# Performance work log

Measured on AMD Instinct MI355X. Metric: run time of the kernel, lower is better.

## Reference

```python
import jax, jax.numpy as jnp
import numpy as np

B, F, O = 32, 26, 20
IN, G = 2048, 512
REL = 53
EPS = 1e-5  # BatchNorm1d default eps


def setup_inputs() -> dict:
    key = jax.random.key(0)
    ks = jax.random.split(key, 10)
    inp = {
        "region_feats": jax.random.normal(ks[0], (B, F, O, IN), jnp.float32),
        "region_masks": jnp.ones((B, F, O), jnp.float32),
        "rel_feats": jax.random.randint(ks[1], (B, F, O, O), 0, REL, jnp.int64),
        "tem_feats": jax.random.uniform(ks[2], (B, F * O, F * O), jnp.float32),
        # learned params (eval mode: dropout off, BN uses running stats)
        "rel_W": jax.random.normal(ks[3], (G, IN), jnp.float32) * (1.0 / np.sqrt(IN)),
        "rel_b": jnp.zeros((G,), jnp.float32),
        "rel_emb": jax.random.normal(ks[4], (REL, G), jnp.float32) * 0.02,
        "tem_W": jax.random.normal(ks[5], (G, IN), jnp.float32) * (1.0 / np.sqrt(IN)),
        "tem_b": jnp.zeros((G,), jnp.float32),
        "bn_w": jnp.ones((F * O,), jnp.float32),
        "bn_b": jnp.zeros((F * O,), jnp.float32),
        "bn_rm": jnp.zeros((F * O,), jnp.float32),
        "bn_rv": jnp.ones((F * O,), jnp.float32),
    }
    return inp


def reference(region_feats, region_masks, rel_feats, tem_feats,
              rel_W, rel_b, rel_emb, tem_W, tem_b,
              bn_w, bn_b, bn_rm, bn_rv):
    b, f, o, _ = region_feats.shape
    # ---- RELATIONAL FEATURE GRAPH ----
    # [B,F,O,G]
    rel_region = jnp.einsum("bfoi,gi->bfog", region_feats, rel_W) + rel_b
    # embedding lookup: [B,F,O,O,G]
    emb = rel_emb[rel_feats]
    mask = (rel_feats > 0).astype(region_feats.dtype)  # [B,F,O,O]
    msum = jnp.sum(mask, axis=3)                        # [B,F,O]
    # sum_j mask_ij * emb_ij  (masked reduction over neighbor dim)
    emb_sum = jnp.einsum("bfijg,bfij->bfig", emb, mask)
    # sum_j mask_ij * r_i == r_i * msum_i, so (emb_sum + r*msum)/msum
    rel_out = (emb_sum + rel_region * msum[..., None]) / msum[..., None]
    rel_out = rel_out.reshape(b, f * o, -1)
    # ---- TEMPORAL FEATURE GRAPH ----
    tem_region = jnp.einsum("bfoi,gi->bfog", region_feats, tem_W) + tem_b
    tem_region = tem_region.reshape(b, f * o, -1)
    tem_sum = jnp.sum(tem_feats, axis=2)                # [B, F*O]
    tem_out = jnp.matmul(tem_feats, tem_region) / tem_sum[..., None]
    # ---- OUTPUT ----
    out = jnp.concatenate([rel_out, tem_out], axis=-1)  # [B, F*O, 2G]
    out = jnp.tanh(out)
    # BatchNorm1d over channel dim 1 (eval mode, running stats)
    inv = bn_w / jnp.sqrt(bn_rv + EPS)                  # [F*O]
    out = (out - bn_rm[None, :, None]) * inv[None, :, None] + bn_b[None, :, None]
    return out
```

## Files before the change

kernel.cpp:

```cpp
#include <hip/hip_runtime.h>
#include <stdint.h>

#define BB 32
#define FO 520
#define M1 16640
#define KIN 2048
#define KA 2112
#define N1 1024
#define GG 512
#define K2P 576
#define M2 640

typedef unsigned short u16;
typedef short v8s __attribute__((ext_vector_type(8)));
typedef float v4f __attribute__((ext_vector_type(4)));

__device__ __forceinline__ u16 f2bf(float f) {
  union { float f; unsigned u; } v; v.f = f;
  unsigned r = v.u + 0x7fffu + ((v.u >> 16) & 1u);
  return (u16)(r >> 16);
}

__device__ __forceinline__ float fast_tanh(float x) {
  float cx = fminf(fmaxf(x, -15.f), 15.f);
  float e = __expf(2.f * cx);
  return (e - 1.f) / (e + 1.f);
}

#define PREP_ROWS 8832
__global__ __launch_bounds__(512) void prep_all_kernel(
    const float* __restrict__ rf, const int* __restrict__ rel,
    const float* __restrict__ relW, const float* __restrict__ temW,
    const float* __restrict__ emb, const float* __restrict__ tem,
    u16* __restrict__ A1, u16* __restrict__ Wc,
    u16* __restrict__ A2, float* __restrict__ tsum) {
  const int blk = blockIdx.x;
  const int t = threadIdx.x;
  if (blk < PREP_ROWS) {
    const int row = blk * 2 + (t >> 8);
    const int tt = t & 255;
    const float* src;
    u16* orow;
    if (row < M1) { src = rf + (size_t)row * KIN; orow = A1 + (size_t)row * KA; }
    else {
      const int n = row - M1;
      src = (n < GG) ? (relW + (size_t)n * KIN) : (temW + (size_t)(n - GG) * KIN);
      orow = Wc + (size_t)n * KA;
    }
    const v4f* p = (const v4f*)src;
    v4f a = __builtin_nontemporal_load(p + 2 * tt);
    v4f b = __builtin_nontemporal_load(p + 2 * tt + 1);
    v8s v;
    v[0] = (short)f2bf(a[0]); v[1] = (short)f2bf(a[1]);
    v[2] = (short)f2bf(a[2]); v[3] = (short)f2bf(a[3]);
    v[4] = (short)f2bf(b[0]); v[5] = (short)f2bf(b[1]);
    v[6] = (short)f2bf(b[2]); v[7] = (short)f2bf(b[3]);
    *(v8s*)(orow + tt * 8) = v;
    if (tt < 64) {
      float sval = 0.f;
      if (row < M1) {
        const int* rp = rel + (size_t)row * 20;
        int cnt = 0, ms = 0;
#pragma unroll
        for (int j = 0; j < 20; ++j) { int ix = rp[j]; cnt += (ix == tt + 1); ms += (ix > 0); }
        if (tt < 52 && ms > 0) sval = (float)cnt / (float)ms;
      } else {
        const int n = row - M1;
        if (n < GG && tt < 52) sval = emb[(size_t)(tt + 1) * GG + n];
      }
      orow[KIN + tt] = f2bf(sval);
    }
    return;
  }
  const int w = t >> 6, l = t & 63;
  const int row = (blk - PREP_ROWS) * 8 + w;
  const int b = row / M2, i = row % M2;
  u16* orow = A2 + (size_t)row * K2P;
  v8s z = {0, 0, 0, 0, 0, 0, 0, 0};
  if (i >= FO) {
    *(v8s*)(orow + l * 8) = z;
    if (l < 8) *(v8s*)(orow + (64 + l) * 8) = z;
    return;
  }
  const float* srow = tem + ((size_t)b * FO + i) * FO;
  float s = 0.f;
  {
    v4f a = __builtin_nontemporal_load((const v4f*)(srow + 8 * l));
    v4f bb = __builtin_nontemporal_load((const v4f*)(srow + 8 * l + 4));
    s += a[0] + a[1] + a[2] + a[3] + bb[0] + bb[1] + bb[2] + bb[3];
    v8s v;
    v[0] = (short)f2bf(a[0]); v[1] = (short)f2bf(a[1]);
    v[2] = (short)f2bf(a[2]); v[3] = (short)f2bf(a[3]);
    v[4] = (short)f2bf(bb[0]); v[5] = (short)f2bf(bb[1]);
    v[6] = (short)f2bf(bb[2]); v[7] = (short)f2bf(bb[3]);
    *(v8s*)(orow + l * 8) = v;
  }
  if (l < 8) {
    if (l == 0) {
      v4f a = __builtin_nontemporal_load((const v4f*)(srow + 512));
      v4f bb = __builtin_nontemporal_load((const v4f*)(srow + 516));
      s += a[0] + a[1] + a[2] + a[3] + bb[0] + bb[1] + bb[2] + bb[3];
      v8s v;
      v[0] = (short)f2bf(a[0]); v[1] = (short)f2bf(a[1]);
      v[2] = (short)f2bf(a[2]); v[3] = (short)f2bf(a[3]);
      v[4] = (short)f2bf(bb[0]); v[5] = (short)f2bf(bb[1]);
      v[6] = (short)f2bf(bb[2]); v[7] = (short)f2bf(bb[3]);
      *(v8s*)(orow + 512) = v;
    } else {
      *(v8s*)(orow + (64 + l) * 8) = z;
    }
  }
#pragma unroll
  for (int off = 32; off > 0; off >>= 1) s += __shfl_down(s, off);
  if (l == 0) tsum[(size_t)b * FO + i] = s;
}

#define G1_STAGE(DST)                                                                            \
  do {                                                                                           \
    u16* dst_ = smem + (DST);                                                                    \
    __builtin_amdgcn_global_load_lds((const __attribute__((address_space(1))) void*)ga0,         \
        (__attribute__((address_space(3))) void*)(dst_ + lofA0), 16, 0, 0);                      \
    __builtin_amdgcn_global_load_lds((const __attribute__((address_space(1))) void*)ga1,         \
        (__attribute__((address_space(3))) void*)(dst_ + lofA1), 16, 0, 0);                      \
    __builtin_amdgcn_global_load_lds((const __attribute__((address_space(1))) void*)gb0,         \
        (__attribute__((address_space(3))) void*)(dst_ + lofB0), 16, 0, 0);                      \
    ga0 += 32; ga1 += 32; gb0 += 32;                                                             \
  } while (0)

#define G1_COMPUTE(CB)                                                                           \
  do {                                                                                           \
    const u16* As_ = smem + (CB) * 12288;                                                        \
    const u16* Bs_ = As_ + 8192;                                                                 \
    v8s af[4], bf[4];                                                                            \
    _Pragma("unroll") for (int t4 = 0; t4 < 4; ++t4) {                                           \
      const int ra = wm * 64 + t4 * 16 + r16;                                                    \
      const int rb = wn * 64 + t4 * 16 + r16;                                                    \
      af[t4] = *(const v8s*)&As_[ra * 32 + ((quad ^ ((ra >> 1) & 3)) * 8)];                      \
      bf[t4] = *(const v8s*)&Bs_[rb * 32 + ((quad ^ ((rb >> 1) & 3)) * 8)];                      \
    }                                                                                            \
    _Pragma("unroll") for (int mtt = 0; mtt < 4; ++mtt)                                          \
      _Pragma("unroll") for (int ntt = 0; ntt < 4; ++ntt)                                        \
        acc[mtt][ntt] =                                                                          \
            __builtin_amdgcn_mfma_f32_16x16x32_bf16(af[mtt], bf[ntt], acc[mtt][ntt], 0, 0, 0);   \
  } while (0)

__global__ __launch_bounds__(512, 4) void gemm1_kernel(
    const u16* __restrict__ A, const u16* __restrict__ Wc,
    const float* __restrict__ rel_b, const float* __restrict__ tem_b,
    const float* __restrict__ bn_w, const float* __restrict__ bn_b,
    const float* __restrict__ bn_rm, const float* __restrict__ bn_rv,
    float* __restrict__ out, u16* __restrict__ BT) {
  __shared__ u16 smem[36864];
  const int tid = threadIdx.x;
  const int lane = tid & 63;
  const int wv = tid >> 6, wm = wv >> 1, wn = wv & 1;
  const int id = blockIdx.x;
  const int wgid = (id & 7) * 65 + (id >> 3);
  const int mt = wgid >> 3, nt = wgid & 7;
  const int m0 = mt * 256, n0 = nt * 128;
  const int quad = lane >> 4, r16 = lane & 15;

  const u16 *ga0, *ga1, *gb0;
  {
    const int r0 = tid >> 2, sl0 = tid & 3;
    ga0 = A + (size_t)(m0 + r0) * KA + (sl0 ^ ((r0 >> 1) & 3)) * 8;
    const int r1 = 128 + (tid >> 2);
    ga1 = A + (size_t)(m0 + r1) * KA + (sl0 ^ ((r1 >> 1) & 3)) * 8;
    gb0 = Wc + (size_t)(n0 + r0) * KA + (sl0 ^ ((r0 >> 1) & 3)) * 8;
  }
  const int lofA0 = wv * 512;
  const int lofA1 = 4096 + wv * 512;
  const int lofB0 = 8192 + wv * 512;

  v4f acc[4][4];
#pragma unroll
  for (int i = 0; i < 4; ++i)
#pragma unroll
    for (int j = 0; j < 4; ++j) { v4f z = {0.f, 0.f, 0.f, 0.f}; acc[i][j] = z; }

  G1_STAGE(0);
  G1_STAGE(12288);

  int cb = 0, nb = 2;
  for (int t = 0; t < 64; ++t) {
    G1_STAGE(nb * 12288);
    asm volatile("s_waitcnt vmcnt(6)" ::: "memory");
    __builtin_amdgcn_s_barrier();
    G1_COMPUTE(cb);
    asm volatile("s_waitcnt lgkmcnt(0)" ::: "memory");
    __builtin_amdgcn_s_barrier();
    cb = (cb == 2) ? 0 : cb + 1;
    nb = (nb == 2) ? 0 : nb + 1;
  }
  {
    const int cb1 = (cb == 2) ? 0 : cb + 1;
    asm volatile("s_waitcnt vmcnt(3)" ::: "memory");
    __builtin_amdgcn_s_barrier();
    G1_COMPUTE(cb);
    asm volatile("s_waitcnt vmcnt(0) lgkmcnt(0)" ::: "memory");
    __builtin_amdgcn_s_barrier();
    G1_COMPUTE(cb1);
  }

  if (n0 < GG) {
#pragma unroll
    for (int mtt = 0; mtt < 4; ++mtt) {
      const int mb = m0 + wm * 64 + mtt * 16 + quad * 4;
      const int bb = mb / FO;
      const int fo0 = mb - bb * FO;
      float inv[4], rm[4], bofs[4];
#pragma unroll
      for (int r = 0; r < 4; ++r) {
        const int fo = fo0 + r;
        inv[r] = bn_w[fo] * rsqrtf(bn_rv[fo] + 1e-5f);
        rm[r] = bn_rm[fo]; bofs[r] = bn_b[fo];
      }
#pragma unroll
      for (int ntt = 0; ntt < 4; ++ntt) {
        const int n = n0 + wn * 64 + ntt * 16 + r16;
        const float rbn = rel_b[n];
#pragma unroll
        for (int r = 0; r < 4; ++r) {
          float val = (fast_tanh(acc[mtt][ntt][r] + rbn) - rm[r]) * inv[r] + bofs[r];
          __builtin_nontemporal_store(val, out + (size_t)(mb + r) * N1 + n);
        }
      }
    }
  } else {
    __syncthreads();
#pragma unroll
    for (int p = 0; p < 2; ++p) {
      if (p) __syncthreads();
      if (wn == p) {
#pragma unroll
        for (int mtt = 0; mtt < 4; ++mtt) {
          const int il = wm * 64 + mtt * 16 + quad * 4;
#pragma unroll
          for (int ntt = 0; ntt < 4; ++ntt) {
            const int gl = ntt * 16 + r16;
            const float tb = tem_b[(n0 - GG) + p * 64 + gl];
            ushort4 w;
            w.x = f2bf(acc[mtt][ntt][0] + tb);
            w.y = f2bf(acc[mtt][ntt][1] + tb);
            w.z = f2bf(acc[mtt][ntt][2] + tb);
            w.w = f2bf(acc[mtt][ntt][3] + tb);
            *(ushort4*)&smem[gl * 264 + il] = w;
          }
        }
      }
      __syncthreads();
#pragma unroll
      for (int pass = 0; pass < 4; ++pass) {
        const int gl = pass * 16 + (tid >> 5);
        const int ch = tid & 31;
        const int m = m0 + ch * 8;
        const int b1 = m / FO;
        const int i1 = m - b1 * FO;
        v8s val = *(const v8s*)&smem[gl * 264 + ch * 8];
        const int g = (n0 - GG) + p * 64 + gl;
        *(v8s*)(BT + ((size_t)(b1 * GG + g)) * K2P + i1) = val;
      }
    }
  }
}

#define G2_STAGE(DST)                                                                            \
  do {                                                                                           \
    u16* dst_ = smem + (DST);                                                                    \
    __builtin_amdgcn_global_load_lds((const __attribute__((address_space(1))) void*)ga0,         \
        (__attribute__((address_space(3))) void*)(dst_ + lofA0), 16, 0, 0);                      \
    __builtin_amdgcn_global_load_lds((const __attribute__((address_space(1))) void*)gb0,         \
        (__attribute__((address_space(3))) void*)(dst_ + lofB0), 16, 0, 0);                      \
    __builtin_amdgcn_global_load_lds((const __attribute__((address_space(1))) void*)ga1,         \
        (__attribute__((address_space(3))) void*)(dst_ + lofA1), 16, 0, 0);                      \
    __builtin_amdgcn_global_load_lds((const __attribute__((address_space(1))) void*)gb1,         \
        (__attribute__((address_space(3))) void*)(dst_ + lofB1), 16, 0, 0);                      \
    ga0 += 32; gb0 += 32; ga1 += 32; gb1 += 32;                                                  \
  } while (0)

#define G2_COMPUTE(CB)                                                                           \
  do {                                                                                           \
    const u16* As_ = smem + (CB) * 8192;                                                         \
    const u16* Bs_ = As_ + 4096;                                                                 \
    v8s af[4], bf[4];                                                                            \
    _Pragma("unroll") for (int t4 = 0; t4 < 4; ++t4) {                                           \
      const int ra = wm * 64 + t4 * 16 + r16;                                                    \
      const int rb = wn * 64 + t4 * 16 + r16;                                                    \
      af[t4] = *(const v8s*)&As_[ra * 32 + ((quad ^ ((ra >> 1) & 3)) * 8)];                      \
      bf[t4] = *(const v8s*)&Bs_[rb * 32 + ((quad ^ ((rb >> 1) & 3)) * 8)];                      \
    }                                                                                            \
    _Pragma("unroll") for (int mtt = 0; mtt < 4; ++mtt)                                          \
      _Pragma("unroll") for (int ntt = 0; ntt < 4; ++ntt)                                        \
        acc[mtt][ntt] =                                                                          \
            __builtin_amdgcn_mfma_f32_16x16x32_bf16(af[mtt], bf[ntt], acc[mtt][ntt], 0, 0, 0);   \
  } while (0)

__global__ __launch_bounds__(256) void gemm2_kernel(
    const u16* __restrict__ A2, const u16* __restrict__ BT,
    const float* __restrict__ tsum,
    const float* __restrict__ bn_w, const float* __restrict__ bn_b,
    const float* __restrict__ bn_rm, const float* __restrict__ bn_rv,
    float* __restrict__ out) {
  __shared__ u16 smem[24576];
  const int tid = threadIdx.x;
  const int lane = tid & 63;
  const int wv = tid >> 6, wm = wv >> 1, wn = wv & 1;
  const int m0 = blockIdx.x * 128;
  const int n0 = blockIdx.y * 128;
  const int b = blockIdx.z;
  const u16* Ab = A2 + (size_t)b * M2 * K2P;
  const u16* Bb = BT + (size_t)b * GG * K2P;
  const int quad = lane >> 4, r16 = lane & 15;

  const u16 *ga0, *ga1, *gb0, *gb1;
  {
    const int r0 = tid >> 2, sl0 = tid & 3;
    const int c0 = sl0 ^ ((r0 >> 1) & 3);
    ga0 = Ab + (size_t)(m0 + r0) * K2P + c0 * 8;
    gb0 = Bb + (size_t)(n0 + r0) * K2P + c0 * 8;
    const int L1 = 256 + tid;
    const int r1 = L1 >> 2, sl1 = L1 & 3;
    const int c1 = sl1 ^ ((r1 >> 1) & 3);
    ga1 = Ab + (size_t)(m0 + r1) * K2P + c1 * 8;
    gb1 = Bb + (size_t)(n0 + r1) * K2P + c1 * 8;
  }
  const int lofA0 = wv * 512, lofA1 = 2048 + wv * 512;
  const int lofB0 = 4096 + wv * 512, lofB1 = 6144 + wv * 512;

  v4f acc[4][4];
#pragma unroll
  for (int i = 0; i < 4; ++i)
#pragma unroll
    for (int j = 0; j < 4; ++j) { v4f z = {0.f, 0.f, 0.f, 0.f}; acc[i][j] = z; }

  G2_STAGE(0);
  G2_STAGE(8192);

  int cb = 0, nb = 2;
  for (int t = 0; t < 16; ++t) {
    G2_STAGE(nb * 8192);
    asm volatile("s_waitcnt vmcnt(8)" ::: "memory");
    __builtin_amdgcn_s_barrier();
    G2_COMPUTE(cb);
    asm volatile("s_waitcnt lgkmcnt(0)" ::: "memory");
    __builtin_amdgcn_s_barrier();
    cb = (cb == 2) ? 0 : cb + 1;
    nb = (nb == 2) ? 0 : nb + 1;
  }
  {
    const int cb1 = (cb == 2) ? 0 : cb + 1;
    asm volatile("s_waitcnt vmcnt(4)" ::: "memory");
    __builtin_amdgcn_s_barrier();
    G2_COMPUTE(cb);
    asm volatile("s_waitcnt vmcnt(0) lgkmcnt(0)" ::: "memory");
    __builtin_amdgcn_s_barrier();
    G2_COMPUTE(cb1);
  }

#pragma unroll
  for (int mtt = 0; mtt < 4; ++mtt) {
    const int ibase = m0 + wm * 64 + mtt * 16 + quad * 4;
    if (ibase >= FO) continue;
    float ts[4], inv[4], rm[4], bofs[4];
#pragma unroll
    for (int r = 0; r < 4; ++r) {
      const int i = ibase + r;
      ts[r] = 1.f / tsum[(size_t)b * FO + i];
      inv[r] = bn_w[i] * rsqrtf(bn_rv[i] + 1e-5f);
      rm[r] = bn_rm[i]; bofs[r] = bn_b[i];
    }
#pragma unroll
    for (int ntt = 0; ntt < 4; ++ntt) {
      const int g = n0 + wn * 64 + ntt * 16 + r16;
#pragma unroll
      for (int r = 0; r < 4; ++r) {
        float val = (fast_tanh(acc[mtt][ntt][r] * ts[r]) - rm[r]) * inv[r] + bofs[r];
        __builtin_nontemporal_store(val, out + ((size_t)(b * FO + (ibase + r))) * N1 + GG + g);
      }
    }
  }
}

extern "C" void kernel_launch(void* const* d_in, const int* in_sizes, int n_in,
                              void* d_out, int out_size, void* d_ws, size_t ws_size,
                              hipStream_t stream) {
  const float* region_feats = (const float*)d_in[0];
  const int* rel_feats = (const int*)d_in[2];
  const float* tem_feats = (const float*)d_in[3];
  const float* rel_W = (const float*)d_in[4];
  const float* rel_b = (const float*)d_in[5];
  const float* rel_emb = (const float*)d_in[6];
  const float* tem_W = (const float*)d_in[7];
  const float* tem_b = (const float*)d_in[8];
  const float* bn_w = (const float*)d_in[9];
  const float* bn_b = (const float*)d_in[10];
  const float* bn_rm = (const float*)d_in[11];
  const float* bn_rv = (const float*)d_in[12];
  float* out = (float*)d_out;

  char* base = (char*)d_ws;
  u16* A1 = (u16*)base;
  u16* Wc = (u16*)(base + 70287360);
  u16* A2 = (u16*)(base + 74612736);
  u16* BT = (u16*)(base + 98205696);
  float* tsum = (float*)(base + 117080064);

  prep_all_kernel<<<PREP_ROWS + 2560, 512, 0, stream>>>(
      region_feats, rel_feats, rel_W, tem_W, rel_emb, tem_feats, A1, Wc, A2, tsum);
  gemm1_kernel<<<520, 512, 0, stream>>>(A1, Wc, rel_b, tem_b,
                                        bn_w, bn_b, bn_rm, bn_rv, out, BT);
  gemm2_kernel<<<dim3(5, 4, 32), 256, 0, stream>>>(A2, BT, tsum,
                                                   bn_w, bn_b, bn_rm, bn_rv, out);
}
```

Baseline: 387.6 us.

## Move temporal prep into gemm1 tail and widen gemm2 tiles to 128x256

The conversion of tem_feats to bf16 and its row sums move out of the prep kernel and into the epilogue of gemm1 blocks, so that work runs after each block's GEMM instead of in a separate phase of the memory-bound prep launch. gemm2 grows to 512 threads with a 128x256 tile, so each A2 tile is loaded once per two B halves, halving A traffic and the block count. The costs are a longer gemm1 tail and larger LDS use per gemm2 block. gemm2 also gets fewer blocks (320), which may reduce occupancy.

```diff
diff --git a/kernel.cpp b/kernel.cpp
--- a/kernel.cpp
+++ b/kernel.cpp
@@ -31,88 +31,43 @@
 __global__ __launch_bounds__(512) void prep_all_kernel(
     const float* __restrict__ rf, const int* __restrict__ rel,
     const float* __restrict__ relW, const float* __restrict__ temW,
-    const float* __restrict__ emb, const float* __restrict__ tem,
-    u16* __restrict__ A1, u16* __restrict__ Wc,
-    u16* __restrict__ A2, float* __restrict__ tsum) {
+    const float* __restrict__ emb,
+    u16* __restrict__ A1, u16* __restrict__ Wc) {
   const int blk = blockIdx.x;
   const int t = threadIdx.x;
-  if (blk < PREP_ROWS) {
-    const int row = blk * 2 + (t >> 8);
-    const int tt = t & 255;
-    const float* src;
-    u16* orow;
-    if (row < M1) { src = rf + (size_t)row * KIN; orow = A1 + (size_t)row * KA; }
-    else {
+  const int row = blk * 2 + (t >> 8);
+  const int tt = t & 255;
+  const float* src;
+  u16* orow;
+  if (row < M1) { src = rf + (size_t)row * KIN; orow = A1 + (size_t)row * KA; }
+  else {
+    const int n = row - M1;
+    src = (n < GG) ? (relW + (size_t)n * KIN) : (temW + (size_t)(n - GG) * KIN);
+    orow = Wc + (size_t)n * KA;
+  }
+  const v4f* p = (const v4f*)src;
+  v4f a = __builtin_nontemporal_load(p + 2 * tt);
+  v4f b = __builtin_nontemporal_load(p + 2 * tt + 1);
+  v8s v;
+  v[0] = (short)f2bf(a[0]); v[1] = (short)f2bf(a[1]);
+  v[2] = (short)f2bf(a[2]); v[3] = (short)f2bf(a[3]);
+  v[4] = (short)f2bf(b[0]); v[5] = (short)f2bf(b[1]);
+  v[6] = (short)f2bf(b[2]); v[7] = (short)f2bf(b[3]);
+  *(v8s*)(orow + tt * 8) = v;
+  if (tt < 64) {
+    float sval = 0.f;
+    if (row < M1) {
+      const int* rp = rel + (size_t)row * 20;
+      int cnt = 0, ms = 0;
+#pragma unroll
+      for (int j = 0; j < 20; ++j) { int ix = rp[j]; cnt += (ix == tt + 1); ms += (ix > 0); }
+      if (tt < 52 && ms > 0) sval = (float)cnt / (float)ms;
+    } else {
       const int n = row - M1;
-      src = (n < GG) ? (relW + (size_t)n * KIN) : (temW + (size_t)(n - GG) * KIN);
-      orow = Wc + (size_t)n * KA;
-    }
-    const v4f* p = (const v4f*)src;
-    v4f a = __builtin_nontemporal_load(p + 2 * tt);
-    v4f b = __builtin_nontemporal_load(p + 2 * tt + 1);
-    v8s v;
-    v[0] = (short)f2bf(a[0]); v[1] = (short)f2bf(a[1]);
-    v[2] = (short)f2bf(a[2]); v[3] = (short)f2bf(a[3]);
-    v[4] = (short)f2bf(b[0]); v[5] = (short)f2bf(b[1]);
-    v[6] = (short)f2bf(b[2]); v[7] = (short)f2bf(b[3]);
-    *(v8s*)(orow + tt * 8) = v;
-    if (tt < 64) {
-      float sval = 0.f;
-      if (row < M1) {
-        const int* rp = rel + (size_t)row * 20;
-        int cnt = 0, ms = 0;
-#pragma unroll
-        for (int j = 0; j < 20; ++j) { int ix = rp[j]; cnt += (ix == tt + 1); ms += (ix > 0); }
-        if (tt < 52 && ms > 0) sval = (float)cnt / (float)ms;
-      } else {
-        const int n = row - M1;
-        if (n < GG && tt < 52) sval = emb[(size_t)(tt + 1) * GG + n];
-      }
-      orow[KIN + tt] = f2bf(sval);
-    }
-    return;
-  }
-  const int w = t >> 6, l = t & 63;
-  const int row = (blk - PREP_ROWS) * 8 + w;
-  const int b = row / M2, i = row % M2;
-  u16* orow = A2 + (size_t)row * K2P;
-  v8s z = {0, 0, 0, 0, 0, 0, 0, 0};
-  if (i >= FO) {
-    *(v8s*)(orow + l * 8) = z;
-    if (l < 8) *(v8s*)(orow + (64 + l) * 8) = z;
-    return;
-  }
-  const float* srow = tem + ((size_t)b * FO + i) * FO;
-  float s = 0.f;
-  {
-    v4f a = __builtin_nontemporal_load((const v4f*)(srow + 8 * l));
-    v4f bb = __builtin_nontemporal_load((const v4f*)(srow + 8 * l + 4));
-    s += a[0] + a[1] + a[2] + a[3] + bb[0] + bb[1] + bb[2] + bb[3];
-    v8s v;
-    v[0] = (short)f2bf(a[0]); v[1] = (short)f2bf(a[1]);
-    v[2] = (short)f2bf(a[2]); v[3] = (short)f2bf(a[3]);
-    v[4] = (short)f2bf(bb[0]); v[5] = (short)f2bf(bb[1]);
-    v[6] = (short)f2bf(bb[2]); v[7] = (short)f2bf(bb[3]);
-    *(v8s*)(orow + l * 8) = v;
-  }
-  if (l < 8) {
-    if (l == 0) {
-      v4f a = __builtin_nontemporal_load((const v4f*)(srow + 512));
-      v4f bb = __builtin_nontemporal_load((const v4f*)(srow + 516));
-      s += a[0] + a[1] + a[2] + a[3] + bb[0] + bb[1] + bb[2] + bb[3];
-      v8s v;
-      v[0] = (short)f2bf(a[0]); v[1] = (short)f2bf(a[1]);
-      v[2] = (short)f2bf(a[2]); v[3] = (short)f2bf(a[3]);
-      v[4] = (short)f2bf(bb[0]); v[5] = (short)f2bf(bb[1]);
-      v[6] = (short)f2bf(bb[2]); v[7] = (short)f2bf(bb[3]);
-      *(v8s*)(orow + 512) = v;
-    } else {
-      *(v8s*)(orow + (64 + l) * 8) = z;
-    }
-  }
-#pragma unroll
-  for (int off = 32; off > 0; off >>= 1) s += __shfl_down(s, off);
-  if (l == 0) tsum[(size_t)b * FO + i] = s;
+      if (n < GG && tt < 52) sval = emb[(size_t)(tt + 1) * GG + n];
+    }
+    orow[KIN + tt] = f2bf(sval);
+  }
 }
 
 #define G1_STAGE(DST)                                                                            \
@@ -149,7 +104,8 @@
     const float* __restrict__ rel_b, const float* __restrict__ tem_b,
     const float* __restrict__ bn_w, const float* __restrict__ bn_b,
     const float* __restrict__ bn_rm, const float* __restrict__ bn_rv,
-    float* __restrict__ out, u16* __restrict__ BT) {
+    float* __restrict__ out, u16* __restrict__ BT,
+    const float* __restrict__ tem, u16* __restrict__ A2, float* __restrict__ tsum) {
   __shared__ u16 smem[36864];
   const int tid = threadIdx.x;
   const int lane = tid & 63;
@@ -262,6 +218,53 @@
       }
     }
   }
+
+  if (id < 512) {
+    const int w = tid >> 6, l = tid & 63;
+#pragma unroll
+    for (int p5 = 0; p5 < 5; ++p5) {
+      const int row = id * 40 + p5 * 8 + w;
+      const int b = row / M2, i = row % M2;
+      u16* orow = A2 + (size_t)row * K2P;
+      v8s z = {0, 0, 0, 0, 0, 0, 0, 0};
+      if (i >= FO) {
+        *(v8s*)(orow + l * 8) = z;
+        if (l < 8) *(v8s*)(orow + (64 + l) * 8) = z;
+        continue;
+      }
+      const float* srow = tem + ((size_t)b * FO + i) * FO;
+      float s = 0.f;
+      {
+        v4f a = __builtin_nontemporal_load((const v4f*)(srow + 8 * l));
+        v4f bb = __builtin_nontemporal_load((const v4f*)(srow + 8 * l + 4));
+        s += a[0] + a[1] + a[2] + a[3] + bb[0] + bb[1] + bb[2] + bb[3];
+        v8s v;
+        v[0] = (short)f2bf(a[0]); v[1] = (short)f2bf(a[1]);
+        v[2] = (short)f2bf(a[2]); v[3] = (short)f2bf(a[3]);
+        v[4] = (short)f2bf(bb[0]); v[5] = (short)f2bf(bb[1]);
+        v[6] = (short)f2bf(bb[2]); v[7] = (short)f2bf(bb[3]);
+        *(v8s*)(orow + l * 8) = v;
+      }
+      if (l < 8) {
+        if (l == 0) {
+          v4f a = __builtin_nontemporal_load((const v4f*)(srow + 512));
+          v4f bb = __builtin_nontemporal_load((const v4f*)(srow + 516));
+          s += a[0] + a[1] + a[2] + a[3] + bb[0] + bb[1] + bb[2] + bb[3];
+          v8s v;
+          v[0] = (short)f2bf(a[0]); v[1] = (short)f2bf(a[1]);
+          v[2] = (short)f2bf(a[2]); v[3] = (short)f2bf(a[3]);
+          v[4] = (short)f2bf(bb[0]); v[5] = (short)f2bf(bb[1]);
+          v[6] = (short)f2bf(bb[2]); v[7] = (short)f2bf(bb[3]);
+          *(v8s*)(orow + 512) = v;
+        } else {
+          *(v8s*)(orow + (64 + l) * 8) = z;
+        }
+      }
+#pragma unroll
+      for (int off = 32; off > 0; off >>= 1) s += __shfl_down(s, off);
+      if (l == 0) tsum[(size_t)b * FO + i] = s;
+    }
+  }
 }
 
 #define G2_STAGE(DST)                                                                            \
@@ -271,16 +274,14 @@
         (__attribute__((address_space(3))) void*)(dst_ + lofA0), 16, 0, 0);                      \
     __builtin_amdgcn_global_load_lds((const __attribute__((address_space(1))) void*)gb0,         \
         (__attribute__((address_space(3))) void*)(dst_ + lofB0), 16, 0, 0);                      \
-    __builtin_amdgcn_global_load_lds((const __attribute__((address_space(1))) void*)ga1,         \
-        (__attribute__((address_space(3))) void*)(dst_ + lofA1), 16, 0, 0);                      \
     __builtin_amdgcn_global_load_lds((const __attribute__((address_space(1))) void*)gb1,         \
         (__attribute__((address_space(3))) void*)(dst_ + lofB1), 16, 0, 0);                      \
-    ga0 += 32; gb0 += 32; ga1 += 32; gb1 += 32;                                                  \
+    ga0 += 32; gb0 += 32; gb1 += 32;                                                             \
   } while (0)
 
 #define G2_COMPUTE(CB)                                                                           \
   do {                                                                                           \
-    const u16* As_ = smem + (CB) * 8192;                                                         \
+    const u16* As_ = smem + (CB) * 12288;                                                        \
     const u16* Bs_ = As_ + 4096;                                                                 \
     v8s af[4], bf[4];                                                                            \
     _Pragma("unroll") for (int t4 = 0; t4 < 4; ++t4) {                                           \
@@ -295,37 +296,34 @@
             __builtin_amdgcn_mfma_f32_16x16x32_bf16(af[mtt], bf[ntt], acc[mtt][ntt], 0, 0, 0);   \
   } while (0)
 
-__global__ __launch_bounds__(256) void gemm2_kernel(
+__global__ __launch_bounds__(512, 4) void gemm2_kernel(
     const u16* __restrict__ A2, const u16* __restrict__ BT,
     const float* __restrict__ tsum,
     const float* __restrict__ bn_w, const float* __restrict__ bn_b,
     const float* __restrict__ bn_rm, const float* __restrict__ bn_rv,
     float* __restrict__ out) {
-  __shared__ u16 smem[24576];
+  __shared__ u16 smem[36864];
   const int tid = threadIdx.x;
   const int lane = tid & 63;
-  const int wv = tid >> 6, wm = wv >> 1, wn = wv & 1;
+  const int wv = tid >> 6, wm = wv >> 2, wn = wv & 3;
   const int m0 = blockIdx.x * 128;
-  const int n0 = blockIdx.y * 128;
+  const int n0 = blockIdx.y * 256;
   const int b = blockIdx.z;
   const u16* Ab = A2 + (size_t)b * M2 * K2P;
   const u16* Bb = BT + (size_t)b * GG * K2P;
   const int quad = lane >> 4, r16 = lane & 15;
 
-  const u16 *ga0, *ga1, *gb0, *gb1;
+  const u16 *ga0, *gb0, *gb1;
   {
     const int r0 = tid >> 2, sl0 = tid & 3;
-    const int c0 = sl0 ^ ((r0 >> 1) & 3);
-    ga0 = Ab + (size_t)(m0 + r0) * K2P + c0 * 8;
-    gb0 = Bb + (size_t)(n0 + r0) * K2P + c0 * 8;
-    const int L1 = 256 + tid;
-    const int r1 = L1 >> 2, sl1 = L1 & 3;
-    const int c1 = sl1 ^ ((r1 >> 1) & 3);
-    ga1 = Ab + (size_t)(m0 + r1) * K2P + c1 * 8;
-    gb1 = Bb + (size_t)(n0 + r1) * K2P + c1 * 8;
-  }
-  const int lofA0 = wv * 512, lofA1 = 2048 + wv * 512;
-  const int lofB0 = 4096 + wv * 512, lofB1 = 6144 + wv * 512;
+    const int c0 = (sl0 ^ ((r0 >> 1) & 3)) * 8;
+    ga0 = Ab + (size_t)(m0 + r0) * K2P + c0;
+    gb0 = Bb + (size_t)(n0 + r0) * K2P + c0;
+    gb1 = Bb + (size_t)(n0 + 128 + r0) * K2P + c0;
+  }
+  const int lofA0 = wv * 512;
+  const int lofB0 = 4096 + wv * 512;
+  const int lofB1 = 8192 + wv * 512;
 
   v4f acc[4][4];
 #pragma unroll
@@ -334,12 +332,12 @@
     for (int j = 0; j < 4; ++j) { v4f z = {0.f, 0.f, 0.f, 0.f}; acc[i][j] = z; }
 
   G2_STAGE(0);
-  G2_STAGE(8192);
+  G2_STAGE(12288);
 
   int cb = 0, nb = 2;
   for (int t = 0; t < 16; ++t) {
-    G2_STAGE(nb * 8192);
-    asm volatile("s_waitcnt vmcnt(8)" ::: "memory");
+    G2_STAGE(nb * 12288);
+    asm volatile("s_waitcnt vmcnt(6)" ::: "memory");
     __builtin_amdgcn_s_barrier();
     G2_COMPUTE(cb);
     asm volatile("s_waitcnt lgkmcnt(0)" ::: "memory");
@@ -349,7 +347,7 @@
   }
   {
     const int cb1 = (cb == 2) ? 0 : cb + 1;
-    asm volatile("s_waitcnt vmcnt(4)" ::: "memory");
+    asm volatile("s_waitcnt vmcnt(3)" ::: "memory");
     __builtin_amdgcn_s_barrier();
     G2_COMPUTE(cb);
     asm volatile("s_waitcnt vmcnt(0) lgkmcnt(0)" ::: "memory");
@@ -405,10 +403,11 @@
   u16* BT = (u16*)(base + 98205696);
   float* tsum = (float*)(base + 117080064);
 
-  prep_all_kernel<<<PREP_ROWS + 2560, 512, 0, stream>>>(
-      region_feats, rel_feats, rel_W, tem_W, rel_emb, tem_feats, A1, Wc, A2, tsum);
+  prep_all_kernel<<<PREP_ROWS, 512, 0, stream>>>(
+      region_feats, rel_feats, rel_W, tem_W, rel_emb, A1, Wc);
   gemm1_kernel<<<520, 512, 0, stream>>>(A1, Wc, rel_b, tem_b,
-                                        bn_w, bn_b, bn_rm, bn_rv, out, BT);
-  gemm2_kernel<<<dim3(5, 4, 32), 256, 0, stream>>>(A2, BT, tsum,
+                                        bn_w, bn_b, bn_rm, bn_rv, out, BT,
+                                        tem_feats, A2, tsum);
+  gemm2_kernel<<<dim3(5, 2, 32), 512, 0, stream>>>(A2, BT, tsum,
                                                    bn_w, bn_b, bn_rm, bn_rv, out);
 }
```

After: 397.5 us. +2.6%, slower.
